# Performance work log

Measured on AMD Instinct MI355X. Metric: run time of the kernel, lower is better.

The kernel has to match this reference:

```python
import jax, jax.numpy as jnp
import numpy as np

NUM_HEADS = 32
NUM_KV_HEADS = 8
HEAD_DIM = 128
N_REP = NUM_HEADS // NUM_KV_HEADS
BLOCK = 256  # kvcache_block_size
NUM_BLOCKS = 32
BATCH = 4
SEQ = 1024
N_TOK = BATCH * SEQ

# scale is computed in the torch module as (1/sqrt(head_dim)) rounded to bfloat16
SCALE = jnp.float32(jnp.asarray(1.0 / np.sqrt(HEAD_DIM), dtype=jnp.bfloat16))


def setup_inputs() -> dict:
    key = jax.random.key(0)
    kq, kk, kv = jax.random.split(key, 3)
    q = jax.random.normal(kq, (N_TOK, NUM_HEADS, HEAD_DIM), dtype=jnp.float32)
    k = jax.random.normal(kk, (N_TOK, NUM_KV_HEADS, HEAD_DIM), dtype=jnp.float32)
    v = jax.random.normal(kv, (N_TOK, NUM_KV_HEADS, HEAD_DIM), dtype=jnp.float32)
    k_cache = jnp.zeros((NUM_BLOCKS, BLOCK, NUM_KV_HEADS, HEAD_DIM), dtype=jnp.float32)
    v_cache = jnp.zeros_like(k_cache)
    slot_mapping = jnp.arange(N_TOK, dtype=jnp.int64 if jax.config.jax_enable_x64 else jnp.int32)
    cu = jnp.arange(BATCH + 1, dtype=jnp.int32) * SEQ
    return {"q": q, "k": k, "v": v, "k_cache": k_cache, "v_cache": v_cache,
            "slot_mapping": slot_mapping, "cu_seqlens_q": cu, "cu_seqlens_k": cu}


def _store_kvcache(k, v, k_cache, v_cache, slot_mapping):
    # scatter store of new K/V into paged cache; invalid slots are dropped
    blk = slot_mapping // BLOCK
    inner = slot_mapping % BLOCK
    valid = (slot_mapping != -1) & (blk < k_cache.shape[0]) & (inner < BLOCK)
    blk = jnp.where(valid, blk, k_cache.shape[0])  # out-of-range -> dropped
    k_cache = k_cache.at[blk, inner].set(k, mode="drop")
    v_cache = v_cache.at[blk, inner].set(v, mode="drop")
    return k_cache, v_cache


def _prefill_attn(q, k, v):
    # packed varlen batch with uniform seq lengths -> dense [B,S,...] causal GQA attention
    qb = q.reshape(BATCH, SEQ, NUM_HEADS, HEAD_DIM)
    kb = jnp.repeat(k.reshape(BATCH, SEQ, NUM_KV_HEADS, HEAD_DIM), N_REP, axis=2)  # repeat_kv
    vb = jnp.repeat(v.reshape(BATCH, SEQ, NUM_KV_HEADS, HEAD_DIM), N_REP, axis=2)
    scores = jnp.einsum("bqhd,bkhd->bhqk", qb, kb) * SCALE  # [B,H,S,S]
    causal = jnp.tril(jnp.ones((SEQ, SEQ), dtype=bool))
    scores = jnp.where(causal, scores, -jnp.inf)
    # torch code clamps to [-100, 100] before softmax (masked -inf becomes -100)
    probs = jax.nn.softmax(jnp.clip(scores, -100.0, 100.0), axis=-1)
    out = jnp.einsum("bhqk,bkhd->bqhd", probs, vb)
    return out.reshape(N_TOK, NUM_HEADS * HEAD_DIM)


def reference(q, k, v, k_cache, v_cache, slot_mapping, cu_seqlens_q, cu_seqlens_k):
    k_cache, v_cache = _store_kvcache(k, v, k_cache, v_cache, slot_mapping)
    o = _prefill_attn(q, k, v)
    return o, k_cache, v_cache
```

## Files before the change

### kernel.cpp

```cpp
#include <hip/hip_runtime.h>
#include <math.h>
#include <string.h>

#define BB 4
#define SS 1024
#define HH 32
#define GG 8
#define DD 128
#define NTOK (BB*SS)
#define NBLK 32
#define BLKSZ 256
#define CACHE_ELEMS ((size_t)NBLK*BLKSZ*GG*DD)

typedef __attribute__((ext_vector_type(8)))  short  short8;
typedef __attribute__((ext_vector_type(16))) float  floatx16;

union FragU { unsigned u[4]; uint4 u4; short8 s8; };

typedef __attribute__((address_space(3))) void  lds_void;
typedef __attribute__((address_space(1))) const void glb_void;

__device__ __forceinline__ unsigned pack_bf16x2(float a, float b) {
    unsigned ua = __builtin_bit_cast(unsigned, a);
    unsigned ub = __builtin_bit_cast(unsigned, b);
    ua = (ua + 0x7FFFu + ((ua >> 16) & 1u)) >> 16;
    ub = (ub + 0x7FFFu + ((ub >> 16) & 1u)) & 0xFFFF0000u;
    return ua | ub;
}

#if __has_builtin(__builtin_amdgcn_permlane32_swap)
#define HAVE_PL32 1
#endif

__device__ __forceinline__ unsigned cvt_pk_bf16(float lo, float hi) {
    unsigned r;
    asm("v_cvt_pk_bf16_f32 %0, %1, %2" : "=v"(r) : "v"(lo), "v"(hi));
    return r;
}

__device__ __forceinline__ float xhalf_max(float x) {
#ifdef HAVE_PL32
    unsigned u = __builtin_bit_cast(unsigned, x);
    auto r = __builtin_amdgcn_permlane32_swap(u, u, false, false);
    return fmaxf(__builtin_bit_cast(float, (unsigned)r[0]),
                 __builtin_bit_cast(float, (unsigned)r[1]));
#else
    return fmaxf(x, __shfl_xor(x, 32));
#endif
}
__device__ __forceinline__ float xhalf_add(float x) {
#ifdef HAVE_PL32
    unsigned u = __builtin_bit_cast(unsigned, x);
    auto r = __builtin_amdgcn_permlane32_swap(u, u, false, false);
    return __builtin_bit_cast(float, (unsigned)r[0]) +
           __builtin_bit_cast(float, (unsigned)r[1]);
#else
    return x + __shfl_xor(x, 32);
#endif
}

__global__ void prep_kv(const float* __restrict__ k, const float* __restrict__ v,
                        const int* __restrict__ slot_mapping,
                        uint4* __restrict__ ksw, uint4* __restrict__ vsw,
                        float* __restrict__ kco, float* __restrict__ vco) {
    __shared__ float lds[32 * 132];
    const int t = threadIdx.x;
    const int kt = blockIdx.x, gy = blockIdx.y, b = blockIdx.z;
    const int isv = gy >> 3, g = gy & 7;
    const float* sp = (isv ? v : k) + ((size_t)(b * SS + kt * 32) * GG + g) * DD;
    float* dco = isv ? vco : kco;
    #pragma unroll
    for (int i = 0; i < 4; ++i) {
        int u = t + 256 * i;
        int row = u >> 5, c4 = u & 31;
        float4 f = *(const float4*)(sp + (size_t)row * (GG * DD) + c4 * 4);
        float* lp = &lds[row * 132 + c4 * 4];
        lp[0] = f.x; lp[1] = f.y; lp[2] = f.z; lp[3] = f.w;
        int slot = slot_mapping[b * SS + kt * 32 + row];
        if ((unsigned)slot < (unsigned)(NBLK * BLKSZ))
            *(float4*)(dco + (size_t)slot * (GG * DD) + g * DD + c4 * 4) = f;
    }
    __syncthreads();
    const int lane = t & 63, hb = lane >> 5, l31 = lane & 31;
    const size_t tbase = ((size_t)(b * GG + g) * 32 + kt) * 8;
    if (!isv) {
        #pragma unroll
        for (int i = 0; i < 2; ++i) {
            int s = (t >> 6) + 4 * i;
            const float* lp = &lds[l31 * 132 + s * 16 + hb * 8];
            uint4 o;
            o.x = pack_bf16x2(lp[0], lp[1]); o.y = pack_bf16x2(lp[2], lp[3]);
            o.z = pack_bf16x2(lp[4], lp[5]); o.w = pack_bf16x2(lp[6], lp[7]);
            ksw[(tbase + s) * 64 + lane] = o;
        }
    } else {
        #pragma unroll
        for (int i = 0; i < 2; ++i) {
            int f8 = (t >> 6) + 4 * i;
            int t4 = f8 >> 1, s2 = f8 & 1;
            int keyb = s2 * 16 + hb * 8;
            int d = t4 * 32 + l31;
            uint4 o;
            o.x = pack_bf16x2(lds[(keyb + 0) * 132 + d], lds[(keyb + 1) * 132 + d]);
            o.y = pack_bf16x2(lds[(keyb + 2) * 132 + d], lds[(keyb + 3) * 132 + d]);
            o.z = pack_bf16x2(lds[(keyb + 4) * 132 + d], lds[(keyb + 5) * 132 + d]);
            o.w = pack_bf16x2(lds[(keyb + 6) * 132 + d], lds[(keyb + 7) * 132 + d]);
            vsw[(tbase + f8) * 64 + lane] = o;
        }
    }
}

__global__ void copy_cache2(const float4* __restrict__ s0, const float4* __restrict__ s1,
                            float4* __restrict__ d0, float4* __restrict__ d1) {
    const size_t half = CACHE_ELEMS / 4;
    size_t i = (size_t)blockIdx.x * 256 + threadIdx.x;
    if (i < half) d0[i] = s0[i];
    else          d1[i - half] = s1[i - half];
}

__global__ __launch_bounds__(256, 2)
void attn_kernel(const float* __restrict__ q,
                 const uint4* __restrict__ ksw,
                 const uint4* __restrict__ vsw,
                 float* __restrict__ out, float sc2 ) {
    __shared__ uint4 sm[2][16][64];
    const int lane = threadIdx.x & 63;
    const int wave = threadIdx.x >> 6;
    const int l31  = lane & 31;
    const int hb   = lane >> 5;

    const int wg  = blockIdx.x;
    const int xcd = wg & 7;
    const int sl  = wg >> 3;
    const int bg  = xcd * 4 + (sl >> 4);
    const int pr  = sl & 15;
    const int b   = bg >> 3, g = bg & 7;
    const int h   = g * 4 + wave;
    const int tb  = b * SS;

    const uint4* kpl = ksw + (size_t)bg * (32 * 8 * 64);
    const uint4* vpl = vsw + (size_t)bg * (32 * 8 * 64);

    #pragma unroll 1
    for (int half = 0; half < 2; ++half) {
        const int qt = half ? pr : (31 - pr);
        const int q0 = qt * 32;

        #pragma unroll
        for (int i = 0; i < 2; ++i) {
            int row = wave * 2 + i;
            __builtin_amdgcn_global_load_lds((glb_void*)(kpl + row * 64 + lane),
                                             (lds_void*)(&sm[0][row][0]),     16, 0, 0);
            __builtin_amdgcn_global_load_lds((glb_void*)(vpl + row * 64 + lane),
                                             (lds_void*)(&sm[0][8 + row][0]), 16, 0, 0);
        }

        short8 qf[8];
        const float* qp = q + ((size_t)(tb + q0 + l31) * HH + h) * DD;
        #pragma unroll
        for (int s = 0; s < 8; ++s) {
            int d0 = s * 16 + hb * 8;
            float4 f0 = *(const float4*)(qp + d0);
            float4 f1 = *(const float4*)(qp + d0 + 4);
            FragU fr;
            fr.u[0] = pack_bf16x2(f0.x, f0.y); fr.u[1] = pack_bf16x2(f0.z, f0.w);
            fr.u[2] = pack_bf16x2(f1.x, f1.y); fr.u[3] = pack_bf16x2(f1.z, f1.w);
            qf[s] = fr.s8;
        }

        floatx16 oacc[4] = {};
        float m = -__builtin_inff(), l = 0.f;

        __syncthreads();

        for (int kt = 0; kt <= qt; ++kt) {
            const int cur = kt & 1;
            if (kt < qt) {
                const uint4* gk = kpl + (kt + 1) * 512;
                const uint4* gv = vpl + (kt + 1) * 512;
                #pragma unroll
                for (int i = 0; i < 2; ++i) {
                    int row = wave * 2 + i;
                    __builtin_amdgcn_global_load_lds((glb_void*)(gk + row * 64 + lane),
                                                     (lds_void*)(&sm[cur ^ 1][row][0]),     16, 0, 0);
                    __builtin_amdgcn_global_load_lds((glb_void*)(gv + row * 64 + lane),
                                                     (lds_void*)(&sm[cur ^ 1][8 + row][0]), 16, 0, 0);
                }
            }
            floatx16 st = {};
            __builtin_amdgcn_s_setprio(1);
            #pragma unroll
            for (int s = 0; s < 8; ++s) {
                FragU ka; ka.u4 = sm[cur][s][lane];
                st = __builtin_amdgcn_mfma_f32_32x32x16_bf16(ka.s8, qf[s], st, 0, 0, 0);
            }
            __builtin_amdgcn_s_setprio(0);

            float e[16];
            #pragma unroll
            for (int r = 0; r < 16; ++r) {
                float val = st[r];
                if (kt == qt) {
                    int row = (r & 3) + 8 * (r >> 2) + 4 * hb;
                    if (row > l31) val = -__builtin_inff();
                }
                e[r] = val;
            }
            float trm[8];
            #pragma unroll
            for (int i = 0; i < 8; ++i) trm[i] = fmaxf(e[i], e[i + 8]);
            #pragma unroll
            for (int i = 0; i < 4; ++i) trm[i] = fmaxf(trm[i], trm[i + 4]);
            float tmax = fmaxf(fmaxf(trm[0], trm[2]), fmaxf(trm[1], trm[3]));
            tmax = xhalf_max(tmax) * sc2;

            if (__any(tmax > m + 8.f)) {
                const float mnew  = fmaxf(m, tmax);
                const float alpha = exp2f(m - mnew);
                #pragma unroll
                for (int t = 0; t < 4; ++t)
                    #pragma unroll
                    for (int r = 0; r < 16; ++r) oacc[t][r] *= alpha;
                l *= alpha;
                m = mnew;
            }

            float p_[16];
            #pragma unroll
            for (int r = 0; r < 16; ++r) p_[r] = exp2f(fmaf(e[r], sc2, -m));
            float sr[8];
            #pragma unroll
            for (int i = 0; i < 8; ++i) sr[i] = p_[i] + p_[i + 8];
            #pragma unroll
            for (int i = 0; i < 4; ++i) sr[i] += sr[i + 4];
            float psum = (sr[0] + sr[1]) + (sr[2] + sr[3]);
            l += xhalf_add(psum);

            unsigned pk[8];
            #pragma unroll
            for (int u2 = 0; u2 < 8; ++u2) pk[u2] = cvt_pk_bf16(p_[2 * u2], p_[2 * u2 + 1]);

            __builtin_amdgcn_s_setprio(1);
            #pragma unroll
            for (int s2 = 0; s2 < 2; ++s2) {
                FragU pf;
#ifdef HAVE_PL32
                auto ra = __builtin_amdgcn_permlane32_swap(pk[4 * s2],     pk[4 * s2 + 2], false, false);
                auto rb = __builtin_amdgcn_permlane32_swap(pk[4 * s2 + 1], pk[4 * s2 + 3], false, false);
                pf.u[0] = (unsigned)ra[0]; pf.u[1] = (unsigned)rb[0];
                pf.u[2] = (unsigned)ra[1]; pf.u[3] = (unsigned)rb[1];
#else
                unsigned px0 = (unsigned)__shfl_xor((int)pk[4 * s2],     32);
                unsigned px1 = (unsigned)__shfl_xor((int)pk[4 * s2 + 1], 32);
                unsigned px2 = (unsigned)__shfl_xor((int)pk[4 * s2 + 2], 32);
                unsigned px3 = (unsigned)__shfl_xor((int)pk[4 * s2 + 3], 32);
                if (hb == 0) { pf.u[0] = pk[4*s2];   pf.u[1] = pk[4*s2+1]; pf.u[2] = px0; pf.u[3] = px1; }
                else         { pf.u[0] = px2; pf.u[1] = px3; pf.u[2] = pk[4*s2+2]; pf.u[3] = pk[4*s2+3]; }
#endif
                #pragma unroll
                for (int t = 0; t < 4; ++t) {
                    FragU vf; vf.u4 = sm[cur][8 + t * 2 + s2][lane];
                    oacc[t] = __builtin_amdgcn_mfma_f32_32x32x16_bf16(vf.s8, pf.s8, oacc[t], 0, 0, 0);
                }
            }
            __builtin_amdgcn_s_setprio(0);
            __syncthreads();
        }

        const float inv_l = 1.f / l;
        float* op = out + ((size_t)(tb + q0 + l31) * HH + h) * DD;
        #pragma unroll
        for (int t = 0; t < 4; ++t) {
            #pragma unroll
            for (int grp = 0; grp < 4; ++grp) {
                float4 o4;
                o4.x = oacc[t][grp * 4 + 0] * inv_l; o4.y = oacc[t][grp * 4 + 1] * inv_l;
                o4.z = oacc[t][grp * 4 + 2] * inv_l; o4.w = oacc[t][grp * 4 + 3] * inv_l;
                *(float4*)(op + t * 32 + grp * 8 + hb * 4) = o4;
            }
        }
    }
}

extern "C" void kernel_launch(void* const* d_in, const int* in_sizes, int n_in,
                              void* d_out, int out_size, void* d_ws, size_t ws_size,
                              hipStream_t stream) {
    const float* q     = (const float*)d_in[0];
    const float* k     = (const float*)d_in[1];
    const float* v     = (const float*)d_in[2];
    const float* kc_in = (const float*)d_in[3];
    const float* vc_in = (const float*)d_in[4];
    const int*   slot  = (const int*)d_in[5];

    float* o_out  = (float*)d_out;
    float* kc_out = o_out + (size_t)NTOK * HH * DD;
    float* vc_out = kc_out + CACHE_ELEMS;

    uint4* ksw = (uint4*)d_ws;
    uint4* vsw = ksw + (size_t)BB * GG * 32 * 8 * 64;

    float sc = 1.0f / sqrtf((float)DD);
    unsigned u; memcpy(&u, &sc, 4);
    u = (u + 0x7FFFu + ((u >> 16) & 1u)) & 0xFFFF0000u;
    memcpy(&sc, &u, 4);
    const float sc2 = sc * 1.44269504088896340736f;

    copy_cache2<<<(int)(CACHE_ELEMS / 4 / 256) * 2, 256, 0, stream>>>(
        (const float4*)kc_in, (const float4*)vc_in, (float4*)kc_out, (float4*)vc_out);
    prep_kv<<<dim3(32, GG * 2, BB), 256, 0, stream>>>(k, v, slot, ksw, vsw, kc_out, vc_out);
    attn_kernel<<<512, 256, 0, stream>>>(q, ksw, vsw, o_out, sc2);
}
```

Before: 311.4 us.

## Process two 32-key tiles per iteration with 64-key LDS double buffer

The attention loop now consumes K/V in 64-key chunks, two 32-key sub-tiles per iteration, with the LDS double buffer doubled to hold them. The online-softmax max/rescale and the per-iteration barrier and prefetch are now amortized over twice as many keys, halving loop iterations and syncs. The cost is more LDS (64KB per block), which may limit occupancy, and more registers for two score tiles. An odd-tile tail is handled with a predicate.

```diff
diff --git a/kernel.cpp b/kernel.cpp
--- a/kernel.cpp
+++ b/kernel.cpp
@@ -57,6 +57,24 @@
 #else
     return x + __shfl_xor(x, 32);
 #endif
+}
+
+__device__ __forceinline__ FragU make_pfrag(const unsigned* pk, int s2, int hb) {
+    FragU pf;
+#ifdef HAVE_PL32
+    auto ra = __builtin_amdgcn_permlane32_swap(pk[4 * s2],     pk[4 * s2 + 2], false, false);
+    auto rb = __builtin_amdgcn_permlane32_swap(pk[4 * s2 + 1], pk[4 * s2 + 3], false, false);
+    pf.u[0] = (unsigned)ra[0]; pf.u[1] = (unsigned)rb[0];
+    pf.u[2] = (unsigned)ra[1]; pf.u[3] = (unsigned)rb[1];
+#else
+    unsigned px0 = (unsigned)__shfl_xor((int)pk[4 * s2],     32);
+    unsigned px1 = (unsigned)__shfl_xor((int)pk[4 * s2 + 1], 32);
+    unsigned px2 = (unsigned)__shfl_xor((int)pk[4 * s2 + 2], 32);
+    unsigned px3 = (unsigned)__shfl_xor((int)pk[4 * s2 + 3], 32);
+    if (hb == 0) { pf.u[0] = pk[4*s2];   pf.u[1] = pk[4*s2+1]; pf.u[2] = px0; pf.u[3] = px1; }
+    else         { pf.u[0] = px2; pf.u[1] = px3; pf.u[2] = pk[4*s2+2]; pf.u[3] = pk[4*s2+3]; }
+#endif
+    return pf;
 }
 
 __global__ void prep_kv(const float* __restrict__ k, const float* __restrict__ v,
@@ -123,7 +141,7 @@
                  const uint4* __restrict__ ksw,
                  const uint4* __restrict__ vsw,
                  float* __restrict__ out, float sc2 ) {
-    __shared__ uint4 sm[2][16][64];
+    __shared__ uint4 sm[2][32][64];
     const int lane = threadIdx.x & 63;
     const int wave = threadIdx.x >> 6;
     const int l31  = lane & 31;
@@ -145,14 +163,15 @@
     for (int half = 0; half < 2; ++half) {
         const int qt = half ? pr : (31 - pr);
         const int q0 = qt * 32;
-
-        #pragma unroll
-        for (int i = 0; i < 2; ++i) {
-            int row = wave * 2 + i;
+        const int nt = (qt >> 1) + 1;
+
+        #pragma unroll
+        for (int i = 0; i < 4; ++i) {
+            int row = wave * 4 + i;
             __builtin_amdgcn_global_load_lds((glb_void*)(kpl + row * 64 + lane),
-                                             (lds_void*)(&sm[0][row][0]),     16, 0, 0);
+                                             (lds_void*)(&sm[0][row][0]),      16, 0, 0);
             __builtin_amdgcn_global_load_lds((glb_void*)(vpl + row * 64 + lane),
-                                             (lds_void*)(&sm[0][8 + row][0]), 16, 0, 0);
+                                             (lds_void*)(&sm[0][16 + row][0]), 16, 0, 0);
         }
 
         short8 qf[8];
@@ -173,42 +192,70 @@
 
         __syncthreads();
 
-        for (int kt = 0; kt <= qt; ++kt) {
-            const int cur = kt & 1;
-            if (kt < qt) {
-                const uint4* gk = kpl + (kt + 1) * 512;
-                const uint4* gv = vpl + (kt + 1) * 512;
-                #pragma unroll
-                for (int i = 0; i < 2; ++i) {
-                    int row = wave * 2 + i;
+        for (int t = 0; t < nt; ++t) {
+            const int cur = t & 1;
+            if (t + 1 < nt) {
+                const uint4* gk = kpl + (t + 1) * 1024;
+                const uint4* gv = vpl + (t + 1) * 1024;
+                #pragma unroll
+                for (int i = 0; i < 4; ++i) {
+                    int row = wave * 4 + i;
                     __builtin_amdgcn_global_load_lds((glb_void*)(gk + row * 64 + lane),
-                                                     (lds_void*)(&sm[cur ^ 1][row][0]),     16, 0, 0);
+                                                     (lds_void*)(&sm[cur ^ 1][row][0]),      16, 0, 0);
                     __builtin_amdgcn_global_load_lds((glb_void*)(gv + row * 64 + lane),
-                                                     (lds_void*)(&sm[cur ^ 1][8 + row][0]), 16, 0, 0);
-                }
-            }
-            floatx16 st = {};
+                                                     (lds_void*)(&sm[cur ^ 1][16 + row][0]), 16, 0, 0);
+                }
+            }
+            const int  tdbl = 2 * t;
+            const bool two  = (tdbl + 1 <= qt);
+            const bool dg0  = (tdbl == qt);
+            const bool dg1  = (tdbl + 1 == qt);
+
+            floatx16 st0 = {}, st1 = {};
             __builtin_amdgcn_s_setprio(1);
             #pragma unroll
             for (int s = 0; s < 8; ++s) {
                 FragU ka; ka.u4 = sm[cur][s][lane];
-                st = __builtin_amdgcn_mfma_f32_32x32x16_bf16(ka.s8, qf[s], st, 0, 0, 0);
+                st0 = __builtin_amdgcn_mfma_f32_32x32x16_bf16(ka.s8, qf[s], st0, 0, 0, 0);
+            }
+            if (two) {
+                #pragma unroll
+                for (int s = 0; s < 8; ++s) {
+                    FragU ka; ka.u4 = sm[cur][8 + s][lane];
+                    st1 = __builtin_amdgcn_mfma_f32_32x32x16_bf16(ka.s8, qf[s], st1, 0, 0, 0);
+                }
             }
             __builtin_amdgcn_s_setprio(0);
 
-            float e[16];
+            float e0[16], e1[16];
             #pragma unroll
             for (int r = 0; r < 16; ++r) {
-                float val = st[r];
-                if (kt == qt) {
+                float v = st0[r];
+                if (dg0) {
                     int row = (r & 3) + 8 * (r >> 2) + 4 * hb;
-                    if (row > l31) val = -__builtin_inff();
-                }
-                e[r] = val;
-            }
+                    if (row > l31) v = -__builtin_inff();
+                }
+                e0[r] = v;
+            }
+            if (two) {
+                #pragma unroll
+                for (int r = 0; r < 16; ++r) {
+                    float v = st1[r];
+                    if (dg1) {
+                        int row = (r & 3) + 8 * (r >> 2) + 4 * hb;
+                        if (row > l31) v = -__builtin_inff();
+                    }
+                    e1[r] = v;
+                }
+            }
+
             float trm[8];
             #pragma unroll
-            for (int i = 0; i < 8; ++i) trm[i] = fmaxf(e[i], e[i + 8]);
+            for (int i = 0; i < 8; ++i) trm[i] = fmaxf(e0[i], e0[i + 8]);
+            if (two) {
+                #pragma unroll
+                for (int i = 0; i < 8; ++i) trm[i] = fmaxf(trm[i], fmaxf(e1[i], e1[i + 8]));
+            }
             #pragma unroll
             for (int i = 0; i < 4; ++i) trm[i] = fmaxf(trm[i], trm[i + 4]);
             float tmax = fmaxf(fmaxf(trm[0], trm[2]), fmaxf(trm[1], trm[3]));
@@ -218,49 +265,58 @@
                 const float mnew  = fmaxf(m, tmax);
                 const float alpha = exp2f(m - mnew);
                 #pragma unroll
-                for (int t = 0; t < 4; ++t)
+                for (int tt = 0; tt < 4; ++tt)
                     #pragma unroll
-                    for (int r = 0; r < 16; ++r) oacc[t][r] *= alpha;
+                    for (int r = 0; r < 16; ++r) oacc[tt][r] *= alpha;
                 l *= alpha;
                 m = mnew;
             }
 
-            float p_[16];
-            #pragma unroll
-            for (int r = 0; r < 16; ++r) p_[r] = exp2f(fmaf(e[r], sc2, -m));
+            #pragma unroll
+            for (int r = 0; r < 16; ++r) e0[r] = exp2f(fmaf(e0[r], sc2, -m));
+            if (two) {
+                #pragma unroll
+                for (int r = 0; r < 16; ++r) e1[r] = exp2f(fmaf(e1[r], sc2, -m));
+            }
             float sr[8];
             #pragma unroll
-            for (int i = 0; i < 8; ++i) sr[i] = p_[i] + p_[i + 8];
+            for (int i = 0; i < 8; ++i) sr[i] = e0[i] + e0[i + 8];
+            if (two) {
+                #pragma unroll
+                for (int i = 0; i < 8; ++i) sr[i] += e1[i] + e1[i + 8];
+            }
             #pragma unroll
             for (int i = 0; i < 4; ++i) sr[i] += sr[i + 4];
             float psum = (sr[0] + sr[1]) + (sr[2] + sr[3]);
             l += xhalf_add(psum);
 
-            unsigned pk[8];
-            #pragma unroll
-            for (int u2 = 0; u2 < 8; ++u2) pk[u2] = cvt_pk_bf16(p_[2 * u2], p_[2 * u2 + 1]);
+            unsigned pk0[8], pk1[8];
+            #pragma unroll
+            for (int u2 = 0; u2 < 8; ++u2) pk0[u2] = cvt_pk_bf16(e0[2 * u2], e0[2 * u2 + 1]);
+            if (two) {
+                #pragma unroll
+                for (int u2 = 0; u2 < 8; ++u2) pk1[u2] = cvt_pk_bf16(e1[2 * u2], e1[2 * u2 + 1]);
+            }
 
             __builtin_amdgcn_s_setprio(1);
             #pragma unroll
             for (int s2 = 0; s2 < 2; ++s2) {
-                FragU pf;
-#ifdef HAVE_PL32
-                auto ra = __builtin_amdgcn_permlane32_swap(pk[4 * s2],     pk[4 * s2 + 2], false, false);
-                auto rb = __builtin_amdgcn_permlane32_swap(pk[4 * s2 + 1], pk[4 * s2 + 3], false, false);
-                pf.u[0] = (unsigned)ra[0]; pf.u[1] = (unsigned)rb[0];
-                pf.u[2] = (unsigned)ra[1]; pf.u[3] = (unsigned)rb[1];
-#else
-                unsigned px0 = (unsigned)__shfl_xor((int)pk[4 * s2],     32);
-                unsigned px1 = (unsigned)__shfl_xor((int)pk[4 * s2 + 1], 32);
-                unsigned px2 = (unsigned)__shfl_xor((int)pk[4 * s2 + 2], 32);
-                unsigned px3 = (unsigned)__shfl_xor((int)pk[4 * s2 + 3], 32);
-                if (hb == 0) { pf.u[0] = pk[4*s2];   pf.u[1] = pk[4*s2+1]; pf.u[2] = px0; pf.u[3] = px1; }
-                else         { pf.u[0] = px2; pf.u[1] = px3; pf.u[2] = pk[4*s2+2]; pf.u[3] = pk[4*s2+3]; }
-#endif
-                #pragma unroll
-                for (int t = 0; t < 4; ++t) {
-                    FragU vf; vf.u4 = sm[cur][8 + t * 2 + s2][lane];
-                    oacc[t] = __builtin_amdgcn_mfma_f32_32x32x16_bf16(vf.s8, pf.s8, oacc[t], 0, 0, 0);
+                FragU pf = make_pfrag(pk0, s2, hb);
+                #pragma unroll
+                for (int t4 = 0; t4 < 4; ++t4) {
+                    FragU vf; vf.u4 = sm[cur][16 + t4 * 2 + s2][lane];
+                    oacc[t4] = __builtin_amdgcn_mfma_f32_32x32x16_bf16(vf.s8, pf.s8, oacc[t4], 0, 0, 0);
+                }
+            }
+            if (two) {
+                #pragma unroll
+                for (int s2 = 0; s2 < 2; ++s2) {
+                    FragU pf = make_pfrag(pk1, s2, hb);
+                    #pragma unroll
+                    for (int t4 = 0; t4 < 4; ++t4) {
+                        FragU vf; vf.u4 = sm[cur][24 + t4 * 2 + s2][lane];
+                        oacc[t4] = __builtin_amdgcn_mfma_f32_32x32x16_bf16(vf.s8, pf.s8, oacc[t4], 0, 0, 0);
+                    }
                 }
             }
             __builtin_amdgcn_s_setprio(0);
@@ -270,13 +326,13 @@
         const float inv_l = 1.f / l;
         float* op = out + ((size_t)(tb + q0 + l31) * HH + h) * DD;
         #pragma unroll
-        for (int t = 0; t < 4; ++t) {
+        for (int t4 = 0; t4 < 4; ++t4) {
             #pragma unroll
             for (int grp = 0; grp < 4; ++grp) {
                 float4 o4;
-                o4.x = oacc[t][grp * 4 + 0] * inv_l; o4.y = oacc[t][grp * 4 + 1] * inv_l;
-                o4.z = oacc[t][grp * 4 + 2] * inv_l; o4.w = oacc[t][grp * 4 + 3] * inv_l;
-                *(float4*)(op + t * 32 + grp * 8 + hb * 4) = o4;
+                o4.x = oacc[t4][grp * 4 + 0] * inv_l; o4.y = oacc[t4][grp * 4 + 1] * inv_l;
+                o4.z = oacc[t4][grp * 4 + 2] * inv_l; o4.w = oacc[t4][grp * 4 + 3] * inv_l;
+                *(float4*)(op + t4 * 32 + grp * 8 + hb * 4) = o4;
             }
         }
     }
```

After: 315.1 us. About the same (+1.2%).

## Load K/V fragments directly into registers instead of staging through LDS

Applied to the files above, without the earlier changes.

The attention kernel no longer stages K/V tiles into shared memory with global_load_lds and block-wide barriers. Each wave now loads its K fragments straight from global memory into registers, double-buffered across iterations by a two-way unrolled loop, and loads V fragments per iteration. This removes the LDS round trip and the __syncthreads per KV tile. In exchange, all four waves (heads sharing a KV group) fetch the same K/V separately, which raises L2 traffic and register pressure (24 extra uint4 registers) and may lower occupancy under launch_bounds(256,2).

```diff
diff --git a/kernel.cpp b/kernel.cpp
--- a/kernel.cpp
+++ b/kernel.cpp
@@ -17,9 +17,6 @@
 
 union FragU { unsigned u[4]; uint4 u4; short8 s8; };
 
-typedef __attribute__((address_space(3))) void  lds_void;
-typedef __attribute__((address_space(1))) const void glb_void;
-
 __device__ __forceinline__ unsigned pack_bf16x2(float a, float b) {
     unsigned ua = __builtin_bit_cast(unsigned, a);
     unsigned ub = __builtin_bit_cast(unsigned, b);
@@ -57,6 +54,24 @@
 #else
     return x + __shfl_xor(x, 32);
 #endif
+}
+
+__device__ __forceinline__ FragU make_pfrag(const unsigned* pk, int s2, int hb) {
+    FragU pf;
+#ifdef HAVE_PL32
+    auto ra = __builtin_amdgcn_permlane32_swap(pk[4 * s2],     pk[4 * s2 + 2], false, false);
+    auto rb = __builtin_amdgcn_permlane32_swap(pk[4 * s2 + 1], pk[4 * s2 + 3], false, false);
+    pf.u[0] = (unsigned)ra[0]; pf.u[1] = (unsigned)rb[0];
+    pf.u[2] = (unsigned)ra[1]; pf.u[3] = (unsigned)rb[1];
+#else
+    unsigned px0 = (unsigned)__shfl_xor((int)pk[4 * s2],     32);
+    unsigned px1 = (unsigned)__shfl_xor((int)pk[4 * s2 + 1], 32);
+    unsigned px2 = (unsigned)__shfl_xor((int)pk[4 * s2 + 2], 32);
+    unsigned px3 = (unsigned)__shfl_xor((int)pk[4 * s2 + 3], 32);
+    if (hb == 0) { pf.u[0] = pk[4*s2];   pf.u[1] = pk[4*s2+1]; pf.u[2] = px0; pf.u[3] = px1; }
+    else         { pf.u[0] = px2; pf.u[1] = px3; pf.u[2] = pk[4*s2+2]; pf.u[3] = pk[4*s2+3]; }
+#endif
+    return pf;
 }
 
 __global__ void prep_kv(const float* __restrict__ k, const float* __restrict__ v,
@@ -123,7 +138,6 @@
                  const uint4* __restrict__ ksw,
                  const uint4* __restrict__ vsw,
                  float* __restrict__ out, float sc2 ) {
-    __shared__ uint4 sm[2][16][64];
     const int lane = threadIdx.x & 63;
     const int wave = threadIdx.x >> 6;
     const int l31  = lane & 31;
@@ -138,22 +152,13 @@
     const int h   = g * 4 + wave;
     const int tb  = b * SS;
 
-    const uint4* kpl = ksw + (size_t)bg * (32 * 8 * 64);
-    const uint4* vpl = vsw + (size_t)bg * (32 * 8 * 64);
+    const uint4* kln = ksw + (size_t)bg * (32 * 8 * 64) + lane;
+    const uint4* vln = vsw + (size_t)bg * (32 * 8 * 64) + lane;
 
     #pragma unroll 1
     for (int half = 0; half < 2; ++half) {
         const int qt = half ? pr : (31 - pr);
         const int q0 = qt * 32;
-
-        #pragma unroll
-        for (int i = 0; i < 2; ++i) {
-            int row = wave * 2 + i;
-            __builtin_amdgcn_global_load_lds((glb_void*)(kpl + row * 64 + lane),
-                                             (lds_void*)(&sm[0][row][0]),     16, 0, 0);
-            __builtin_amdgcn_global_load_lds((glb_void*)(vpl + row * 64 + lane),
-                                             (lds_void*)(&sm[0][8 + row][0]), 16, 0, 0);
-        }
 
         short8 qf[8];
         const float* qp = q + ((size_t)(tb + q0 + l31) * HH + h) * DD;
@@ -171,27 +176,23 @@
         floatx16 oacc[4] = {};
         float m = -__builtin_inff(), l = 0.f;
 
-        __syncthreads();
-
-        for (int kt = 0; kt <= qt; ++kt) {
-            const int cur = kt & 1;
+        uint4 kA[8], kB[8], vv[8];
+        #pragma unroll
+        for (int s = 0; s < 8; ++s) kA[s] = kln[s * 64];
+
+        auto body = [&](uint4 (&kc)[8], uint4 (&kn)[8], int kt) {
             if (kt < qt) {
-                const uint4* gk = kpl + (kt + 1) * 512;
-                const uint4* gv = vpl + (kt + 1) * 512;
                 #pragma unroll
-                for (int i = 0; i < 2; ++i) {
-                    int row = wave * 2 + i;
-                    __builtin_amdgcn_global_load_lds((glb_void*)(gk + row * 64 + lane),
-                                                     (lds_void*)(&sm[cur ^ 1][row][0]),     16, 0, 0);
-                    __builtin_amdgcn_global_load_lds((glb_void*)(gv + row * 64 + lane),
-                                                     (lds_void*)(&sm[cur ^ 1][8 + row][0]), 16, 0, 0);
-                }
-            }
+                for (int s = 0; s < 8; ++s) kn[s] = kln[(kt + 1) * 512 + s * 64];
+            }
+            #pragma unroll
+            for (int s = 0; s < 8; ++s) vv[s] = vln[kt * 512 + s * 64];
+
             floatx16 st = {};
             __builtin_amdgcn_s_setprio(1);
             #pragma unroll
             for (int s = 0; s < 8; ++s) {
-                FragU ka; ka.u4 = sm[cur][s][lane];
+                FragU ka; ka.u4 = kc[s];
                 st = __builtin_amdgcn_mfma_f32_32x32x16_bf16(ka.s8, qf[s], st, 0, 0, 0);
             }
             __builtin_amdgcn_s_setprio(0);
@@ -199,12 +200,12 @@
             float e[16];
             #pragma unroll
             for (int r = 0; r < 16; ++r) {
-                float val = st[r];
+                float v = st[r];
                 if (kt == qt) {
                     int row = (r & 3) + 8 * (r >> 2) + 4 * hb;
-                    if (row > l31) val = -__builtin_inff();
+                    if (row > l31) v = -__builtin_inff();
                 }
-                e[r] = val;
+                e[r] = v;
             }
             float trm[8];
             #pragma unroll
@@ -218,19 +219,18 @@
                 const float mnew  = fmaxf(m, tmax);
                 const float alpha = exp2f(m - mnew);
                 #pragma unroll
-                for (int t = 0; t < 4; ++t)
+                for (int tt = 0; tt < 4; ++tt)
                     #pragma unroll
-                    for (int r = 0; r < 16; ++r) oacc[t][r] *= alpha;
+                    for (int r = 0; r < 16; ++r) oacc[tt][r] *= alpha;
                 l *= alpha;
                 m = mnew;
             }
 
-            float p_[16];
-            #pragma unroll
-            for (int r = 0; r < 16; ++r) p_[r] = exp2f(fmaf(e[r], sc2, -m));
+            #pragma unroll
+            for (int r = 0; r < 16; ++r) e[r] = exp2f(fmaf(e[r], sc2, -m));
             float sr[8];
             #pragma unroll
-            for (int i = 0; i < 8; ++i) sr[i] = p_[i] + p_[i + 8];
+            for (int i = 0; i < 8; ++i) sr[i] = e[i] + e[i + 8];
             #pragma unroll
             for (int i = 0; i < 4; ++i) sr[i] += sr[i + 4];
             float psum = (sr[0] + sr[1]) + (sr[2] + sr[3]);
@@ -238,45 +238,40 @@
 
             unsigned pk[8];
             #pragma unroll
-            for (int u2 = 0; u2 < 8; ++u2) pk[u2] = cvt_pk_bf16(p_[2 * u2], p_[2 * u2 + 1]);
+            for (int u2 = 0; u2 < 8; ++u2) pk[u2] = cvt_pk_bf16(e[2 * u2], e[2 * u2 + 1]);
 
             __builtin_amdgcn_s_setprio(1);
             #pragma unroll
             for (int s2 = 0; s2 < 2; ++s2) {
-                FragU pf;
-#ifdef HAVE_PL32
-                auto ra = __builtin_amdgcn_permlane32_swap(pk[4 * s2],     pk[4 * s2 + 2], false, false);
-                auto rb = __builtin_amdgcn_permlane32_swap(pk[4 * s2 + 1], pk[4 * s2 + 3], false, false);
-                pf.u[0] = (unsigned)ra[0]; pf.u[1] = (unsigned)rb[0];
-                pf.u[2] = (unsigned)ra[1]; pf.u[3] = (unsigned)rb[1];
-#else
-                unsigned px0 = (unsigned)__shfl_xor((int)pk[4 * s2],     32);
-                unsigned px1 = (unsigned)__shfl_xor((int)pk[4 * s2 + 1], 32);
-                unsigned px2 = (unsigned)__shfl_xor((int)pk[4 * s2 + 2], 32);
-                unsigned px3 = (unsigned)__shfl_xor((int)pk[4 * s2 + 3], 32);
-                if (hb == 0) { pf.u[0] = pk[4*s2];   pf.u[1] = pk[4*s2+1]; pf.u[2] = px0; pf.u[3] = px1; }
-                else         { pf.u[0] = px2; pf.u[1] = px3; pf.u[2] = pk[4*s2+2]; pf.u[3] = pk[4*s2+3]; }
-#endif
+                FragU pf = make_pfrag(pk, s2, hb);
                 #pragma unroll
-                for (int t = 0; t < 4; ++t) {
-                    FragU vf; vf.u4 = sm[cur][8 + t * 2 + s2][lane];
-                    oacc[t] = __builtin_amdgcn_mfma_f32_32x32x16_bf16(vf.s8, pf.s8, oacc[t], 0, 0, 0);
+                for (int t4 = 0; t4 < 4; ++t4) {
+                    FragU vf; vf.u4 = vv[t4 * 2 + s2];
+                    oacc[t4] = __builtin_amdgcn_mfma_f32_32x32x16_bf16(vf.s8, pf.s8, oacc[t4], 0, 0, 0);
                 }
             }
             __builtin_amdgcn_s_setprio(0);
-            __syncthreads();
+        };
+
+        int kt = 0;
+        #pragma unroll 1
+        for (;;) {
+            body(kA, kB, kt);
+            if (++kt > qt) break;
+            body(kB, kA, kt);
+            if (++kt > qt) break;
         }
 
         const float inv_l = 1.f / l;
         float* op = out + ((size_t)(tb + q0 + l31) * HH + h) * DD;
         #pragma unroll
-        for (int t = 0; t < 4; ++t) {
+        for (int t4 = 0; t4 < 4; ++t4) {
             #pragma unroll
             for (int grp = 0; grp < 4; ++grp) {
                 float4 o4;
-                o4.x = oacc[t][grp * 4 + 0] * inv_l; o4.y = oacc[t][grp * 4 + 1] * inv_l;
-                o4.z = oacc[t][grp * 4 + 2] * inv_l; o4.w = oacc[t][grp * 4 + 3] * inv_l;
-                *(float4*)(op + t * 32 + grp * 8 + hb * 4) = o4;
+                o4.x = oacc[t4][grp * 4 + 0] * inv_l; o4.y = oacc[t4][grp * 4 + 1] * inv_l;
+                o4.z = oacc[t4][grp * 4 + 2] * inv_l; o4.w = oacc[t4][grp * 4 + 3] * inv_l;
+                *(float4*)(op + t4 * 32 + grp * 8 + hb * 4) = o4;
             }
         }
     }
```

Result: no change. 314.3 us (+0.9%).
